# Kernel tuning notes

Measured on AMD Instinct MI355X. Metric: run time of the kernel, lower is better.

## Reference

```python
import jax, jax.numpy as jnp
import numpy as np

N_NODES = 20000
N_EDGES = 320000
N_ADJ = 4
D = 256
CSTR = [0, 1]          # constrained adjacency subset for the last step
RATIO = 1.0
LN_EPS = 1e-5


def setup_inputs() -> dict:
    key = jax.random.key(0)
    ks = jax.random.split(key, 10)
    x = jax.random.normal(ks[0], (N_NODES, D), dtype=jnp.float32)
    rows = jax.random.randint(ks[1], (N_ADJ, N_EDGES), 0, N_NODES)
    cols = jax.random.randint(ks[2], (N_ADJ, N_EDGES), 0, N_NODES)
    vals = jax.random.uniform(ks[3], (N_ADJ, N_EDGES), dtype=jnp.float32)
    W = jax.random.normal(ks[4], (D, D), dtype=jnp.float32) * (1.0 / np.sqrt(D))
    b = jax.random.normal(ks[5], (D,), dtype=jnp.float32) * 0.02
    ws_seq_0 = jax.random.uniform(ks[6], (2, N_ADJ - 1), dtype=jnp.float32)
    ws_seq_1 = jax.random.uniform(ks[7], (len(CSTR),), dtype=jnp.float32)
    ws_res_0 = jax.random.uniform(ks[8], (1, N_ADJ), dtype=jnp.float32)
    ws_res_1 = jax.random.uniform(ks[9], (2, len(CSTR) + 1), dtype=jnp.float32)
    return {"x": x, "rows": rows, "cols": cols, "vals": vals, "W": W, "b": b,
            "ws_seq_0": ws_seq_0, "ws_seq_1": ws_seq_1,
            "ws_res_0": ws_res_0, "ws_res_1": ws_res_1}


def reference(x, rows, cols, vals, W, b, ws_seq_0, ws_seq_1, ws_res_0, ws_res_1):
    n_nodes = x.shape[0]

    def spmm(a, h):
        # sparse [n,n] @ h : gather source features, scale, scatter-add by row
        return jax.ops.segment_sum(vals[a][:, None] * h[cols[a]], rows[a],
                                   num_segments=n_nodes)

    def op(h, adj_ids, w):
        # Op with k=1: random.sample selects ALL operators -> weighted mean
        acc = w[0] * spmm(adj_ids[0], h)
        for j, a in enumerate(adj_ids[1:], start=1):
            acc = acc + w[j] * spmm(a, h)
        return acc / len(adj_ids)

    h = x @ W + b                      # affine: [n_nodes, D]
    states = [h]
    # step i=0: seq only (res sum over states[:0] is empty -> 0), edge == 1
    s1 = op(states[0], [0, 1, 2], ws_seq_0[0])          # adjs[:-1]
    states.append(s1)
    # step i=1: seq on states[1] over adjs[:-1], res on states[0] over all adjs
    s2 = op(states[1], [0, 1, 2], ws_seq_0[1]) + RATIO * op(states[0], [0, 1, 2, 3], ws_res_0[0])
    states.append(s2)
    # last step: cstr adjacencies for seq; cstr + last adj for residuals
    out_seq = op(states[2], CSTR, ws_seq_1)
    res_ids = CSTR + [N_ADJ - 1]
    out_res = op(states[0], res_ids, ws_res_1[0]) + op(states[1], res_ids, ws_res_1[1])
    out = out_seq + RATIO * out_res
    # LayerNorm without affine params
    mu = jnp.mean(out, axis=-1, keepdims=True)
    var = jnp.var(out, axis=-1, keepdims=True)
    out = (out - mu) * jax.lax.rsqrt(var + LN_EPS)
    return jax.nn.gelu(out, approximate=False)
```

## Files before the change

kernel.cpp:

```cpp
#include <hip/hip_runtime.h>
#include <hip/hip_bf16.h>

#define N_NODES 20000
#define N_EDGES 320000
#define N_ADJ   4
#define D       256
#define DH      128
#define RPA     20004

#define NBUCK   79
#define NGRP    40
#define EPB     8000
#define GCAP    192
#define BMAX    4736
#define MMBLK   1250

typedef __attribute__((ext_vector_type(8))) short bf8;
typedef __attribute__((ext_vector_type(4))) float f4;


__device__ __forceinline__ unsigned f2bf_bits(float x) {
    unsigned u = __float_as_uint(x);
    return (u + 0x7FFFu + ((u >> 16) & 1u)) >> 16;
}
__device__ __forceinline__ unsigned pack_bf2(float lo, float hi) {
    return f2bf_bits(lo) | (f2bf_bits(hi) << 16);
}
__device__ __forceinline__ float bf_lo(unsigned p) { return __uint_as_float(p << 16); }
__device__ __forceinline__ float bf_hi(unsigned p) { return __uint_as_float(p & 0xFFFF0000u); }


__global__ __launch_bounds__(1024) void prep_kernel(const int* __restrict__ rows,
                                                    const int* __restrict__ cols,
                                                    const float* __restrict__ vals,
                                                    int* __restrict__ cnt,
                                                    uint2* __restrict__ stage,
                                                    const float* __restrict__ W,
                                                    uint4* __restrict__ wh,
                                                    uint4* __restrict__ wl) {
    __shared__ int lcnt[NBUCK];
    int g = blockIdx.x, a = blockIdx.y, t = threadIdx.x;

    if (g >= NGRP) {
        if (a != 0) return;
        for (int i = (g - NGRP) * 1024 + t; i < 8192; i += 2048) {
            int lane = i & 63;
            int tile = i >> 6;
            int ks = tile >> 4, n = tile & 15;
            int m = lane & 15, quad = lane >> 4;
            int col = n * 16 + m;
            int k0  = ks * 32 + quad * 8;
            unsigned hbits[8], lbits[8];
            #pragma unroll
            for (int j = 0; j < 8; ++j) {
                float v = W[(k0 + j) * D + col];
                unsigned hb = f2bf_bits(v);
                float lo = v - __uint_as_float(hb << 16);
                hbits[j] = hb;
                lbits[j] = f2bf_bits(lo);
            }
            uint4 hh, ll;
            hh.x = hbits[0] | (hbits[1] << 16); hh.y = hbits[2] | (hbits[3] << 16);
            hh.z = hbits[4] | (hbits[5] << 16); hh.w = hbits[6] | (hbits[7] << 16);
            ll.x = lbits[0] | (lbits[1] << 16); ll.y = lbits[2] | (lbits[3] << 16);
            ll.z = lbits[4] | (lbits[5] << 16); ll.w = lbits[6] | (lbits[7] << 16);
            wh[i] = hh;
            wl[i] = ll;
        }
        return;
    }

    if (t < NBUCK) lcnt[t] = 0;
    __syncthreads();
    int e0 = g * EPB;
    #pragma unroll 1
    for (int i = 0; i < EPB; i += 1024) {
        int e = e0 + i + t;
        if (i + t < EPB) {
            int r   = rows[a * N_EDGES + e];
            int c   = cols[a * N_EDGES + e];
            float v = vals[a * N_EDGES + e];
            int b   = r >> 8;
            int idx = atomicAdd(&lcnt[b], 1);
            if (idx < GCAP) {
                stage[(size_t)((a * NBUCK + b) * NGRP + g) * GCAP + idx] =
                    make_uint2((f2bf_bits(v) << 16) | (unsigned)c, (unsigned)(r & 255));
            }
        }
    }
    __syncthreads();
    if (t < NBUCK) cnt[(a * NBUCK + t) * NGRP + g] = min(lcnt[t], GCAP);
}


__global__ __launch_bounds__(256) void buildmm_kernel(const float* __restrict__ x,
                                                      const uint4* __restrict__ wh,
                                                      const uint4* __restrict__ wl,
                                                      const float* __restrict__ bvec,
                                                      unsigned* __restrict__ hp,
                                                      const int* __restrict__ cnt,
                                                      const uint2* __restrict__ stage,
                                                      unsigned* __restrict__ csr,
                                                      int* __restrict__ row_ptr) {
    __shared__ uint2 recs[BMAX];
    __shared__ int scn[256];
    __shared__ int offs[256];
    __shared__ int gbase_s;
    int t = threadIdx.x;

    if (blockIdx.x < MMBLK) {
        int wid = t >> 6, lane = t & 63;
        int r0 = blockIdx.x * 16;
        int m = lane & 15, quad = lane >> 4;

        const float* xr = x + (size_t)(r0 + m) * D + quad * 8;
        bf8 ah[8], al[8];
        #pragma unroll
        for (int ks = 0; ks < 8; ++ks) {
            float4 v0 = *(const float4*)(xr + ks * 32);
            float4 v1 = *(const float4*)(xr + ks * 32 + 4);
            float xs[8] = {v0.x, v0.y, v0.z, v0.w, v1.x, v1.y, v1.z, v1.w};
            #pragma unroll
            for (int j = 0; j < 8; ++j) {
                unsigned hb = f2bf_bits(xs[j]);
                float lo = xs[j] - __uint_as_float(hb << 16);
                ah[ks][j] = (short)hb;
                al[ks][j] = (short)f2bf_bits(lo);
            }
        }

        #pragma unroll
        for (int i = 0; i < 4; ++i) {
            int n = wid * 4 + i;
            f4 c = {0.f, 0.f, 0.f, 0.f};
            #pragma unroll
            for (int ks = 0; ks < 8; ++ks) {
                uint4 bh4 = wh[(ks * 16 + n) * 64 + lane];
                uint4 bl4 = wl[(ks * 16 + n) * 64 + lane];
                bf8 bh = *(bf8*)&bh4;
                bf8 bl = *(bf8*)&bl4;
                c = __builtin_amdgcn_mfma_f32_16x16x32_bf16(ah[ks], bh, c, 0, 0, 0);
                c = __builtin_amdgcn_mfma_f32_16x16x32_bf16(al[ks], bh, c, 0, 0, 0);
                c = __builtin_amdgcn_mfma_f32_16x16x32_bf16(ah[ks], bl, c, 0, 0, 0);
            }
            int col = n * 16 + m;
            float bb = bvec[col];
            #pragma unroll
            for (int reg = 0; reg < 4; ++reg) {
                float v = c[reg] + bb;
                float o = __shfl_xor(v, 1, 64);
                if ((m & 1) == 0) {
                    hp[(r0 + quad * 4 + reg) * DH + (col >> 1)] = pack_bf2(v, o);
                }
            }
        }
        return;
    }

    int linear = blockIdx.x - MMBLK;
    int a = linear / NBUCK, b = linear % NBUCK;

    if (t == 0) gbase_s = 0;
    __syncthreads();
    int part = 0;
    for (int i = t; i < b * NGRP; i += 256) part += cnt[a * (NBUCK * NGRP) + i];
    #pragma unroll
    for (int off = 32; off > 0; off >>= 1) part += __shfl_xor(part, off, 64);
    if ((t & 63) == 0) atomicAdd(&gbase_s, part);

    int goff = 0;
    #pragma unroll 1
    for (int g = 0; g < NGRP; ++g) {
        int c = cnt[(a * NBUCK + b) * NGRP + g];
        const uint2* src = stage + (size_t)((a * NBUCK + b) * NGRP + g) * GCAP;
        for (int i = t; i < c; i += 256) {
            int d = goff + i;
            if (d < BMAX) recs[d] = src[i];
        }
        goff += c;
    }
    int total = min(goff, BMAX);

    scn[t] = 0;
    offs[t] = 0;
    __syncthreads();
    for (int i = t; i < total; i += 256) atomicAdd(&scn[recs[i].y], 1);
    __syncthreads();
    int mycnt = scn[t];
    for (int off = 1; off < 256; off <<= 1) {
        int add = (t >= off) ? scn[t - off] : 0;
        __syncthreads();
        scn[t] += add;
        __syncthreads();
    }
    int excl = scn[t] - mycnt;
    __syncthreads();
    scn[t] = excl;
    __syncthreads();

    int gbase = gbase_s;
    for (int i = t; i < total; i += 256) {
        int lr  = recs[i].y;
        int pos = scn[lr] + atomicAdd(&offs[lr], 1);
        csr[(size_t)a * N_EDGES + gbase + pos] = recs[i].x;
    }
    int r = b * 256 + t;
    if (r <= N_NODES) row_ptr[(size_t)a * RPA + r] = gbase + excl;
}


__device__ __forceinline__ void gather_seg(const unsigned* __restrict__ E, int beg, int end,
                                           const uint2* __restrict__ feat2, int lane,
                                           float* __restrict__ s ) {
    int n = end - beg;
    const unsigned* e = E + beg;
    int m8 = n & ~7;
    if (m8) {
        unsigned rec[8];
        #pragma unroll
        for (int j = 0; j < 8; ++j) rec[j] = e[j];
        for (int i = 8; ; i += 8) {
            uint2 p[8];
            #pragma unroll
            for (int j = 0; j < 8; ++j)
                p[j] = feat2[((rec[j] & 0xFFFFu) << 6) + lane];
            bool more = i < m8;
            unsigned nrec[8];
            if (more) {
                #pragma unroll
                for (int j = 0; j < 8; ++j) nrec[j] = e[i + j];
            }
            #pragma unroll
            for (int j = 0; j < 8; ++j) {
                float v = __uint_as_float(rec[j] & 0xFFFF0000u);
                s[0] += v * bf_lo(p[j].x);
                s[1] += v * bf_hi(p[j].x);
                s[2] += v * bf_lo(p[j].y);
                s[3] += v * bf_hi(p[j].y);
            }
            if (!more) break;
            #pragma unroll
            for (int j = 0; j < 8; ++j) rec[j] = nrec[j];
        }
    }
    for (int i = m8; i < n; ++i) {
        unsigned rr = e[i];
        uint2 pp = feat2[((rr & 0xFFFFu) << 6) + lane];
        float vv = __uint_as_float(rr & 0xFFFF0000u);
        s[0] += vv * bf_lo(pp.x);
        s[1] += vv * bf_hi(pp.x);
        s[2] += vv * bf_lo(pp.y);
        s[3] += vv * bf_hi(pp.y);
    }
}


__global__ __launch_bounds__(256) void stage1_kernel(const uint2* __restrict__ hp2,
                                                     const int* __restrict__ row_ptr,
                                                     const unsigned* __restrict__ csr,
                                                     const float* __restrict__ wseq0,
                                                     const float* __restrict__ wres0,
                                                     const float* __restrict__ wres1,
                                                     uint2* __restrict__ s1p2,
                                                     uint2* __restrict__ s2p2,
                                                     float4* __restrict__ outp4) {
    int t = threadIdx.x, wid = t >> 6, lane = t & 63;
    int r = blockIdx.x * 4 + wid;
    float acc[N_ADJ][4];
    #pragma unroll
    for (int a = 0; a < N_ADJ; ++a) {
        acc[a][0] = acc[a][1] = acc[a][2] = acc[a][3] = 0.f;
        const int* rp = row_ptr + (size_t)a * RPA;
        int beg = __builtin_amdgcn_readfirstlane(rp[r]);
        int end = __builtin_amdgcn_readfirstlane(rp[r + 1]);
        gather_seg(csr + (size_t)a * N_EDGES, beg, end, hp2, lane, acc[a]);
    }
    const float third = 1.f / 3.f;
    float w0 = wseq0[0] * third, w1 = wseq0[1] * third, w2 = wseq0[2] * third;
    float q0 = wres0[0] * 0.25f, q1 = wres0[1] * 0.25f, q2 = wres0[2] * 0.25f, q3 = wres0[3] * 0.25f;
    float u0 = wres1[0] * third, u1 = wres1[1] * third, u2 = wres1[2] * third;
    float s1v[4], s2v[4], ov[4];
    #pragma unroll
    for (int j = 0; j < 4; ++j) {
        s1v[j] = w0 * acc[0][j] + w1 * acc[1][j] + w2 * acc[2][j];
        s2v[j] = q0 * acc[0][j] + q1 * acc[1][j] + q2 * acc[2][j] + q3 * acc[3][j];
        ov[j]  = u0 * acc[0][j] + u1 * acc[1][j] + u2 * acc[3][j];
    }
    int o = r * 64 + lane;
    s1p2[o]  = make_uint2(pack_bf2(s1v[0], s1v[1]), pack_bf2(s1v[2], s1v[3]));
    s2p2[o]  = make_uint2(pack_bf2(s2v[0], s2v[1]), pack_bf2(s2v[2], s2v[3]));
    outp4[o] = make_float4(ov[0], ov[1], ov[2], ov[3]);
}


__global__ __launch_bounds__(256) void stage2_kernel(const uint2* __restrict__ s1p2,
                                                     const int* __restrict__ row_ptr,
                                                     const unsigned* __restrict__ csr,
                                                     const float* __restrict__ wseq0,
                                                     const float* __restrict__ wres1,
                                                     uint2* __restrict__ s2p2,
                                                     float4* __restrict__ outp4) {
    int t = threadIdx.x, wid = t >> 6, lane = t & 63;
    int r = blockIdx.x * 4 + wid;
    float acc[N_ADJ][4];
    #pragma unroll
    for (int a = 0; a < N_ADJ; ++a) {
        acc[a][0] = acc[a][1] = acc[a][2] = acc[a][3] = 0.f;
        const int* rp = row_ptr + (size_t)a * RPA;
        int beg = __builtin_amdgcn_readfirstlane(rp[r]);
        int end = __builtin_amdgcn_readfirstlane(rp[r + 1]);
        gather_seg(csr + (size_t)a * N_EDGES, beg, end, s1p2, lane, acc[a]);
    }
    const float third = 1.f / 3.f;
    float w3 = wseq0[3] * third, w4 = wseq0[4] * third, w5 = wseq0[5] * third;
    float u3 = wres1[3] * third, u4 = wres1[4] * third, u5 = wres1[5] * third;
    int o = r * 64 + lane;
    uint2 sp = s2p2[o];
    float c0 = bf_lo(sp.x) + w3 * acc[0][0] + w4 * acc[1][0] + w5 * acc[2][0];
    float c1 = bf_hi(sp.x) + w3 * acc[0][1] + w4 * acc[1][1] + w5 * acc[2][1];
    float c2 = bf_lo(sp.y) + w3 * acc[0][2] + w4 * acc[1][2] + w5 * acc[2][2];
    float c3 = bf_hi(sp.y) + w3 * acc[0][3] + w4 * acc[1][3] + w5 * acc[2][3];
    s2p2[o] = make_uint2(pack_bf2(c0, c1), pack_bf2(c2, c3));
    float4 op = outp4[o];
    op.x += u3 * acc[0][0] + u4 * acc[1][0] + u5 * acc[3][0];
    op.y += u3 * acc[0][1] + u4 * acc[1][1] + u5 * acc[3][1];
    op.z += u3 * acc[0][2] + u4 * acc[1][2] + u5 * acc[3][2];
    op.w += u3 * acc[0][3] + u4 * acc[1][3] + u5 * acc[3][3];
    outp4[o] = op;
}


__global__ __launch_bounds__(256) void stage3_kernel(const uint2* __restrict__ s2p2,
                                                     const int* __restrict__ row_ptr,
                                                     const unsigned* __restrict__ csr,
                                                     const float* __restrict__ wseq1,
                                                     float4* __restrict__ outp4) {
    int t = threadIdx.x, wid = t >> 6, lane = t & 63;
    int r = blockIdx.x * 4 + wid;
    float acc[2][4];
    #pragma unroll
    for (int a = 0; a < 2; ++a) {
        acc[a][0] = acc[a][1] = acc[a][2] = acc[a][3] = 0.f;
        const int* rp = row_ptr + (size_t)a * RPA;
        int beg = __builtin_amdgcn_readfirstlane(rp[r]);
        int end = __builtin_amdgcn_readfirstlane(rp[r + 1]);
        gather_seg(csr + (size_t)a * N_EDGES, beg, end, s2p2, lane, acc[a]);
    }
    float e0 = wseq1[0] * 0.5f, e1 = wseq1[1] * 0.5f;
    int o = r * 64 + lane;
    float4 op = outp4[o];
    float v0 = op.x + e0 * acc[0][0] + e1 * acc[1][0];
    float v1 = op.y + e0 * acc[0][1] + e1 * acc[1][1];
    float v2 = op.z + e0 * acc[0][2] + e1 * acc[1][2];
    float v3 = op.w + e0 * acc[0][3] + e1 * acc[1][3];

    float sv = v0 + v1 + v2 + v3;
    float sq = v0 * v0 + v1 * v1 + v2 * v2 + v3 * v3;
    #pragma unroll
    for (int off = 32; off > 0; off >>= 1) {
        sv += __shfl_xor(sv, off, 64);
        sq += __shfl_xor(sq, off, 64);
    }
    float mu   = sv * (1.f / 256.f);
    float var  = sq * (1.f / 256.f) - mu * mu;
    float rstd = rsqrtf(var + 1e-5f);
    float y0 = (v0 - mu) * rstd;
    float y1 = (v1 - mu) * rstd;
    float y2 = (v2 - mu) * rstd;
    float y3 = (v3 - mu) * rstd;
    const float is2 = 0.70710678118654752440f;
    outp4[o] = make_float4(0.5f * y0 * (1.f + erff(y0 * is2)),
                           0.5f * y1 * (1.f + erff(y1 * is2)),
                           0.5f * y2 * (1.f + erff(y2 * is2)),
                           0.5f * y3 * (1.f + erff(y3 * is2)));
}


extern "C" void kernel_launch(void* const* d_in, const int* in_sizes, int n_in,
                              void* d_out, int out_size, void* d_ws, size_t ws_size,
                              hipStream_t stream) {
    const float* x     = (const float*)d_in[0];
    const int*   rows  = (const int*)d_in[1];
    const int*   cols  = (const int*)d_in[2];
    const float* vals  = (const float*)d_in[3];
    const float* W     = (const float*)d_in[4];
    const float* b     = (const float*)d_in[5];
    const float* wseq0 = (const float*)d_in[6];
    const float* wseq1 = (const float*)d_in[7];
    const float* wres0 = (const float*)d_in[8];
    const float* wres1 = (const float*)d_in[9];
    float4* outp4 = (float4*)d_out;

    char* p = (char*)d_ws;
    unsigned* hp  = (unsigned*)p; p += (size_t)N_NODES * DH * 4;
    unsigned* s1p = (unsigned*)p; p += (size_t)N_NODES * DH * 4;
    unsigned* s2p = (unsigned*)p; p += (size_t)N_NODES * DH * 4;
    int* row_ptr  = (int*)p;      p += (size_t)N_ADJ * RPA * 4;
    int* cnt      = (int*)p;      p += (N_ADJ * NBUCK * NGRP * 4 + 127) / 128 * 128;
    uint4* wh     = (uint4*)p;    p += 8192 * 16;
    uint4* wl     = (uint4*)p;    p += 8192 * 16;
    unsigned* csr = (unsigned*)p;
    uint2* stage  = (uint2*)s1p;

    prep_kernel<<<dim3(NGRP + 2, N_ADJ), 1024, 0, stream>>>(rows, cols, vals, cnt,
                                                            stage, W, wh, wl);
    buildmm_kernel<<<MMBLK + NBUCK * N_ADJ, 256, 0, stream>>>(x, wh, wl, b, hp,
                                                              cnt, stage, csr, row_ptr);

    stage1_kernel<<<N_NODES / 4, 256, 0, stream>>>((const uint2*)hp, row_ptr, csr,
                                                   wseq0, wres0, wres1,
                                                   (uint2*)s1p, (uint2*)s2p, outp4);
    stage2_kernel<<<N_NODES / 4, 256, 0, stream>>>((const uint2*)s1p, row_ptr, csr,
                                                   wseq0, wres1, (uint2*)s2p, outp4);
    stage3_kernel<<<N_NODES / 4, 256, 0, stream>>>((const uint2*)s2p, row_ptr, csr,
                                                   wseq1, outp4);
}
```

Baseline: 329.3 us.

## Sub-sort CSR rows by source-column quarter and gather quarter-by-quarter across adjacencies

New measurement: 352.8 us. 1.07x slower.

```diff
diff --git a/kernel.cpp b/kernel.cpp
--- a/kernel.cpp
+++ b/kernel.cpp
@@ -6,7 +6,7 @@
 #define N_ADJ   4
 #define D       256
 #define DH      128
-#define RPA     20004
+#define RP4A    80016
 
 #define NBUCK   79
 #define NGRP    40
@@ -15,8 +15,11 @@
 #define BMAX    4736
 #define MMBLK   1250
 
+#define GD      4
+
 typedef __attribute__((ext_vector_type(8))) short bf8;
 typedef __attribute__((ext_vector_type(4))) float f4;
+typedef __attribute__((ext_vector_type(2))) unsigned u2v;
 
 
 __device__ __forceinline__ unsigned f2bf_bits(float x) {
@@ -83,8 +86,10 @@
             int b   = r >> 8;
             int idx = atomicAdd(&lcnt[b], 1);
             if (idx < GCAP) {
+                unsigned q = (unsigned)((c >= 5000) + (c >= 10000) + (c >= 15000));
                 stage[(size_t)((a * NBUCK + b) * NGRP + g) * GCAP + idx] =
-                    make_uint2((f2bf_bits(v) << 16) | (unsigned)c, (unsigned)(r & 255));
+                    make_uint2((f2bf_bits(v) << 16) | (unsigned)c,
+                               (unsigned)((r & 255) * 4) + q);
             }
         }
     }
@@ -101,10 +106,11 @@
                                                       const int* __restrict__ cnt,
                                                       const uint2* __restrict__ stage,
                                                       unsigned* __restrict__ csr,
-                                                      int* __restrict__ row_ptr) {
+                                                      int* __restrict__ rp4) {
     __shared__ uint2 recs[BMAX];
-    __shared__ int scn[256];
-    __shared__ int offs[256];
+    __shared__ int scn[1024];
+    __shared__ int offs[1024];
+    __shared__ int tscan[256];
     __shared__ int gbase_s;
     int t = threadIdx.x;
 
@@ -181,82 +187,91 @@
     }
     int total = min(goff, BMAX);
 
-    scn[t] = 0;
-    offs[t] = 0;
+    #pragma unroll
+    for (int k = 0; k < 4; ++k) { scn[t * 4 + k] = 0; offs[t * 4 + k] = 0; }
     __syncthreads();
     for (int i = t; i < total; i += 256) atomicAdd(&scn[recs[i].y], 1);
     __syncthreads();
-    int mycnt = scn[t];
+    int c0 = scn[t * 4], c1 = scn[t * 4 + 1], c2 = scn[t * 4 + 2], c3 = scn[t * 4 + 3];
+    int tsum = c0 + c1 + c2 + c3;
+    tscan[t] = tsum;
+    __syncthreads();
     for (int off = 1; off < 256; off <<= 1) {
-        int add = (t >= off) ? scn[t - off] : 0;
+        int add = (t >= off) ? tscan[t - off] : 0;
         __syncthreads();
-        scn[t] += add;
+        tscan[t] += add;
         __syncthreads();
     }
-    int excl = scn[t] - mycnt;
-    __syncthreads();
-    scn[t] = excl;
+    int texcl = tscan[t] - tsum;
+    int e0 = texcl, e1 = e0 + c0, e2 = e1 + c1, e3 = e2 + c2;
+    scn[t * 4] = e0; scn[t * 4 + 1] = e1; scn[t * 4 + 2] = e2; scn[t * 4 + 3] = e3;
     __syncthreads();
 
     int gbase = gbase_s;
     for (int i = t; i < total; i += 256) {
-        int lr  = recs[i].y;
-        int pos = scn[lr] + atomicAdd(&offs[lr], 1);
+        int key = recs[i].y;
+        int pos = scn[key] + atomicAdd(&offs[key], 1);
         csr[(size_t)a * N_EDGES + gbase + pos] = recs[i].x;
     }
     int r = b * 256 + t;
-    if (r <= N_NODES) row_ptr[(size_t)a * RPA + r] = gbase + excl;
+    if (r <= N_NODES) {
+        rp4[(size_t)a * RP4A + r * 4 + 0] = gbase + e0;
+        rp4[(size_t)a * RP4A + r * 4 + 1] = gbase + e1;
+        rp4[(size_t)a * RP4A + r * 4 + 2] = gbase + e2;
+        rp4[(size_t)a * RP4A + r * 4 + 3] = gbase + e3;
+    }
 }
 
 
 __device__ __forceinline__ void gather_seg(const unsigned* __restrict__ E, int beg, int end,
-                                           const uint2* __restrict__ feat2, int lane,
+                                           const uint2* __restrict__ feat2, int lo8 ,
                                            float* __restrict__ s ) {
     int n = end - beg;
+    if (n <= 0) return;
     const unsigned* e = E + beg;
-    int m8 = n & ~7;
-    if (m8) {
-        unsigned rec[8];
-        #pragma unroll
-        for (int j = 0; j < 8; ++j) rec[j] = e[j];
-        for (int i = 8; ; i += 8) {
-            uint2 p[8];
+    int lim = n - 1;
+    unsigned rec[GD];
+    #pragma unroll
+    for (int j = 0; j < GD; ++j) rec[j] = e[min(j, lim)];
+    int base = 0;
+    #pragma unroll 1
+    for (;;) {
+        u2v p[GD];
+        #pragma unroll
+        for (int j = 0; j < GD; ++j) {
+            unsigned voff = ((rec[j] & 0xFFFFu) << 9) + (unsigned)lo8;
+            asm volatile("global_load_dwordx2 %0, %1, %2"
+                         : "=v"(p[j])
+                         : "v"(voff), "s"(feat2));
+        }
+        int nbase = base + GD;
+        bool more = nbase < n;
+        unsigned nrec[GD];
+        if (more) {
             #pragma unroll
-            for (int j = 0; j < 8; ++j)
-                p[j] = feat2[((rec[j] & 0xFFFFu) << 6) + lane];
-            bool more = i < m8;
-            unsigned nrec[8];
-            if (more) {
-                #pragma unroll
-                for (int j = 0; j < 8; ++j) nrec[j] = e[i + j];
-            }
-            #pragma unroll
-            for (int j = 0; j < 8; ++j) {
-                float v = __uint_as_float(rec[j] & 0xFFFF0000u);
-                s[0] += v * bf_lo(p[j].x);
-                s[1] += v * bf_hi(p[j].x);
-                s[2] += v * bf_lo(p[j].y);
-                s[3] += v * bf_hi(p[j].y);
-            }
-            if (!more) break;
-            #pragma unroll
-            for (int j = 0; j < 8; ++j) rec[j] = nrec[j];
-        }
-    }
-    for (int i = m8; i < n; ++i) {
-        unsigned rr = e[i];
-        uint2 pp = feat2[((rr & 0xFFFFu) << 6) + lane];
-        float vv = __uint_as_float(rr & 0xFFFF0000u);
-        s[0] += vv * bf_lo(pp.x);
-        s[1] += vv * bf_hi(pp.x);
-        s[2] += vv * bf_lo(pp.y);
-        s[3] += vv * bf_hi(pp.y);
+            for (int j = 0; j < GD; ++j) nrec[j] = e[min(nbase + j, lim)];
+        }
+        asm volatile("s_waitcnt vmcnt(0)"
+                     : "+v"(p[0]), "+v"(p[1]), "+v"(p[2]), "+v"(p[3]));
+        #pragma unroll
+        for (int j = 0; j < GD; ++j) {
+            unsigned vb = (base + j <= lim) ? (rec[j] & 0xFFFF0000u) : 0u;
+            float v = __uint_as_float(vb);
+            s[0] += v * bf_lo(p[j][0]);
+            s[1] += v * bf_hi(p[j][0]);
+            s[2] += v * bf_lo(p[j][1]);
+            s[3] += v * bf_hi(p[j][1]);
+        }
+        if (!more) break;
+        #pragma unroll
+        for (int j = 0; j < GD; ++j) rec[j] = nrec[j];
+        base = nbase;
     }
 }
 
 
 __global__ __launch_bounds__(256) void stage1_kernel(const uint2* __restrict__ hp2,
-                                                     const int* __restrict__ row_ptr,
+                                                     const int* __restrict__ rp4,
                                                      const unsigned* __restrict__ csr,
                                                      const float* __restrict__ wseq0,
                                                      const float* __restrict__ wres0,
@@ -266,15 +281,25 @@
                                                      float4* __restrict__ outp4) {
     int t = threadIdx.x, wid = t >> 6, lane = t & 63;
     int r = blockIdx.x * 4 + wid;
+    int lo8 = lane * 8;
+    int rps[N_ADJ][5];
+    #pragma unroll
+    for (int a = 0; a < N_ADJ; ++a)
+        #pragma unroll
+        for (int k = 0; k < 5; ++k)
+            rps[a][k] = __builtin_amdgcn_readfirstlane(rp4[(size_t)a * RP4A + r * 4 + k]);
+
     float acc[N_ADJ][4];
     #pragma unroll
-    for (int a = 0; a < N_ADJ; ++a) {
+    for (int a = 0; a < N_ADJ; ++a)
         acc[a][0] = acc[a][1] = acc[a][2] = acc[a][3] = 0.f;
-        const int* rp = row_ptr + (size_t)a * RPA;
-        int beg = __builtin_amdgcn_readfirstlane(rp[r]);
-        int end = __builtin_amdgcn_readfirstlane(rp[r + 1]);
-        gather_seg(csr + (size_t)a * N_EDGES, beg, end, hp2, lane, acc[a]);
-    }
+
+    #pragma unroll
+    for (int q = 0; q < 4; ++q)
+        #pragma unroll
+        for (int a = 0; a < N_ADJ; ++a)
+            gather_seg(csr + (size_t)a * N_EDGES, rps[a][q], rps[a][q + 1], hp2, lo8, acc[a]);
+
     const float third = 1.f / 3.f;
     float w0 = wseq0[0] * third, w1 = wseq0[1] * third, w2 = wseq0[2] * third;
     float q0 = wres0[0] * 0.25f, q1 = wres0[1] * 0.25f, q2 = wres0[2] * 0.25f, q3 = wres0[3] * 0.25f;
@@ -294,7 +319,7 @@
 
 
 __global__ __launch_bounds__(256) void stage2_kernel(const uint2* __restrict__ s1p2,
-                                                     const int* __restrict__ row_ptr,
+                                                     const int* __restrict__ rp4,
                                                      const unsigned* __restrict__ csr,
                                                      const float* __restrict__ wseq0,
                                                      const float* __restrict__ wres1,
@@ -302,15 +327,25 @@
                                                      float4* __restrict__ outp4) {
     int t = threadIdx.x, wid = t >> 6, lane = t & 63;
     int r = blockIdx.x * 4 + wid;
+    int lo8 = lane * 8;
+    int rps[N_ADJ][5];
+    #pragma unroll
+    for (int a = 0; a < N_ADJ; ++a)
+        #pragma unroll
+        for (int k = 0; k < 5; ++k)
+            rps[a][k] = __builtin_amdgcn_readfirstlane(rp4[(size_t)a * RP4A + r * 4 + k]);
+
     float acc[N_ADJ][4];
     #pragma unroll
-    for (int a = 0; a < N_ADJ; ++a) {
+    for (int a = 0; a < N_ADJ; ++a)
         acc[a][0] = acc[a][1] = acc[a][2] = acc[a][3] = 0.f;
-        const int* rp = row_ptr + (size_t)a * RPA;
-        int beg = __builtin_amdgcn_readfirstlane(rp[r]);
-        int end = __builtin_amdgcn_readfirstlane(rp[r + 1]);
-        gather_seg(csr + (size_t)a * N_EDGES, beg, end, s1p2, lane, acc[a]);
-    }
+
+    #pragma unroll
+    for (int q = 0; q < 4; ++q)
+        #pragma unroll
+        for (int a = 0; a < N_ADJ; ++a)
+            gather_seg(csr + (size_t)a * N_EDGES, rps[a][q], rps[a][q + 1], s1p2, lo8, acc[a]);
+
     const float third = 1.f / 3.f;
     float w3 = wseq0[3] * third, w4 = wseq0[4] * third, w5 = wseq0[5] * third;
     float u3 = wres1[3] * third, u4 = wres1[4] * third, u5 = wres1[5] * third;
@@ -331,21 +366,31 @@
 
 
 __global__ __launch_bounds__(256) void stage3_kernel(const uint2* __restrict__ s2p2,
-                                                     const int* __restrict__ row_ptr,
+                                                     const int* __restrict__ rp4,
                                                      const unsigned* __restrict__ csr,
                                                      const float* __restrict__ wseq1,
                                                      float4* __restrict__ outp4) {
     int t = threadIdx.x, wid = t >> 6, lane = t & 63;
     int r = blockIdx.x * 4 + wid;
+    int lo8 = lane * 8;
+    int rps[2][5];
+    #pragma unroll
+    for (int a = 0; a < 2; ++a)
+        #pragma unroll
+        for (int k = 0; k < 5; ++k)
+            rps[a][k] = __builtin_amdgcn_readfirstlane(rp4[(size_t)a * RP4A + r * 4 + k]);
+
     float acc[2][4];
     #pragma unroll
-    for (int a = 0; a < 2; ++a) {
+    for (int a = 0; a < 2; ++a)
         acc[a][0] = acc[a][1] = acc[a][2] = acc[a][3] = 0.f;
-        const int* rp = row_ptr + (size_t)a * RPA;
-        int beg = __builtin_amdgcn_readfirstlane(rp[r]);
-        int end = __builtin_amdgcn_readfirstlane(rp[r + 1]);
-        gather_seg(csr + (size_t)a * N_EDGES, beg, end, s2p2, lane, acc[a]);
-    }
+
+    #pragma unroll
+    for (int q = 0; q < 4; ++q)
+        #pragma unroll
+        for (int a = 0; a < 2; ++a)
+            gather_seg(csr + (size_t)a * N_EDGES, rps[a][q], rps[a][q + 1], s2p2, lo8, acc[a]);
+
     float e0 = wseq1[0] * 0.5f, e1 = wseq1[1] * 0.5f;
     int o = r * 64 + lane;
     float4 op = outp4[o];
@@ -395,7 +440,7 @@
     unsigned* hp  = (unsigned*)p; p += (size_t)N_NODES * DH * 4;
     unsigned* s1p = (unsigned*)p; p += (size_t)N_NODES * DH * 4;
     unsigned* s2p = (unsigned*)p; p += (size_t)N_NODES * DH * 4;
-    int* row_ptr  = (int*)p;      p += (size_t)N_ADJ * RPA * 4;
+    int* rp4      = (int*)p;      p += (size_t)N_ADJ * RP4A * 4;
     int* cnt      = (int*)p;      p += (N_ADJ * NBUCK * NGRP * 4 + 127) / 128 * 128;
     uint4* wh     = (uint4*)p;    p += 8192 * 16;
     uint4* wl     = (uint4*)p;    p += 8192 * 16;
@@ -405,13 +450,13 @@
     prep_kernel<<<dim3(NGRP + 2, N_ADJ), 1024, 0, stream>>>(rows, cols, vals, cnt,
                                                             stage, W, wh, wl);
     buildmm_kernel<<<MMBLK + NBUCK * N_ADJ, 256, 0, stream>>>(x, wh, wl, b, hp,
-                                                              cnt, stage, csr, row_ptr);
-
-    stage1_kernel<<<N_NODES / 4, 256, 0, stream>>>((const uint2*)hp, row_ptr, csr,
+                                                              cnt, stage, csr, rp4);
+
+    stage1_kernel<<<N_NODES / 4, 256, 0, stream>>>((const uint2*)hp, rp4, csr,
                                                    wseq0, wres0, wres1,
                                                    (uint2*)s1p, (uint2*)s2p, outp4);
-    stage2_kernel<<<N_NODES / 4, 256, 0, stream>>>((const uint2*)s1p, row_ptr, csr,
+    stage2_kernel<<<N_NODES / 4, 256, 0, stream>>>((const uint2*)s1p, rp4, csr,
                                                    wseq0, wres1, (uint2*)s2p, outp4);
-    stage3_kernel<<<N_NODES / 4, 256, 0, stream>>>((const uint2*)s2p, row_ptr, csr,
+    stage3_kernel<<<N_NODES / 4, 256, 0, stream>>>((const uint2*)s2p, rp4, csr,
                                                    wseq1, outp4);
 }
```

## Split feature tables into column planes and gather per plane with quarter-wave edges

Applied to the files above, without the earlier changes.

Measured after the change: 454.7 us. 38.1% more time.

```diff
diff --git a/kernel.cpp b/kernel.cpp
--- a/kernel.cpp
+++ b/kernel.cpp
@@ -7,6 +7,8 @@
 #define D       256
 #define DH      128
 #define RPA     20004
+#define PLANE_DW 640000
+#define PLANE_U2 320000
 
 #define NBUCK   79
 #define NGRP    40
@@ -150,7 +152,10 @@
                 float v = c[reg] + bb;
                 float o = __shfl_xor(v, 1, 64);
                 if ((m & 1) == 0) {
-                    hp[(r0 + quad * 4 + reg) * DH + (col >> 1)] = pack_bf2(v, o);
+                    int pl = col >> 6;
+                    int dw = (col >> 1) & 31;
+                    hp[(size_t)pl * PLANE_DW + (r0 + quad * 4 + reg) * 32 + dw] =
+                        pack_bf2(v, o);
                 }
             }
         }
@@ -209,63 +214,48 @@
 }
 
 
-__device__ __forceinline__ void gather_seg(const unsigned* __restrict__ E, int beg, int end,
-                                           const uint2* __restrict__ feat2, int lane,
-                                           float* __restrict__ s ) {
+__device__ __forceinline__ void gather_q(const unsigned* __restrict__ e, int beg, int end,
+                                         const unsigned* __restrict__ plane,
+                                         int sub, int fl, float* __restrict__ s) {
     int n = end - beg;
-    const unsigned* e = E + beg;
-    int m8 = n & ~7;
-    if (m8) {
-        unsigned rec[8];
-        #pragma unroll
-        for (int j = 0; j < 8; ++j) rec[j] = e[j];
-        for (int i = 8; ; i += 8) {
-            uint2 p[8];
-            #pragma unroll
-            for (int j = 0; j < 8; ++j)
-                p[j] = feat2[((rec[j] & 0xFFFFu) << 6) + lane];
-            bool more = i < m8;
-            unsigned nrec[8];
-            if (more) {
-                #pragma unroll
-                for (int j = 0; j < 8; ++j) nrec[j] = e[i + j];
-            }
-            #pragma unroll
-            for (int j = 0; j < 8; ++j) {
-                float v = __uint_as_float(rec[j] & 0xFFFF0000u);
-                s[0] += v * bf_lo(p[j].x);
-                s[1] += v * bf_hi(p[j].x);
-                s[2] += v * bf_lo(p[j].y);
-                s[3] += v * bf_hi(p[j].y);
-            }
-            if (!more) break;
-            #pragma unroll
-            for (int j = 0; j < 8; ++j) rec[j] = nrec[j];
-        }
-    }
-    for (int i = m8; i < n; ++i) {
-        unsigned rr = e[i];
-        uint2 pp = feat2[((rr & 0xFFFFu) << 6) + lane];
-        float vv = __uint_as_float(rr & 0xFFFF0000u);
-        s[0] += vv * bf_lo(pp.x);
-        s[1] += vv * bf_hi(pp.x);
-        s[2] += vv * bf_lo(pp.y);
-        s[3] += vv * bf_hi(pp.y);
-    }
-}
-
-
-__global__ __launch_bounds__(256) void stage1_kernel(const uint2* __restrict__ hp2,
+    const unsigned* ee = e + beg;
+    int lim = n - 1;
+    #pragma unroll 2
+    for (int base = 0; base < n; base += 4) {
+        int idx = base + sub;
+        unsigned rec = ee[min(idx, lim)];
+        unsigned vb = (idx <= lim) ? (rec & 0xFFFF0000u) : 0u;
+        float v = __uint_as_float(vb);
+        uint2 p = *((const uint2*)(plane + (size_t)(rec & 0xFFFFu) * 32) + fl);
+        s[0] += v * bf_lo(p.x);
+        s[1] += v * bf_hi(p.x);
+        s[2] += v * bf_lo(p.y);
+        s[3] += v * bf_hi(p.y);
+    }
+}
+
+__device__ __forceinline__ float red4(float v) {
+    v += __shfl_xor(v, 16, 64);
+    v += __shfl_xor(v, 32, 64);
+    return v;
+}
+
+
+__global__ __launch_bounds__(256) void stage1_kernel(const unsigned* __restrict__ hp,
                                                      const int* __restrict__ row_ptr,
                                                      const unsigned* __restrict__ csr,
                                                      const float* __restrict__ wseq0,
                                                      const float* __restrict__ wres0,
                                                      const float* __restrict__ wres1,
-                                                     uint2* __restrict__ s1p2,
-                                                     uint2* __restrict__ s2p2,
-                                                     float4* __restrict__ outp4) {
+                                                     unsigned* __restrict__ s1p,
+                                                     unsigned* __restrict__ s2p,
+                                                     float4* __restrict__ outp4,
+                                                     int q) {
     int t = threadIdx.x, wid = t >> 6, lane = t & 63;
+    int sub = lane >> 4, fl = lane & 15;
     int r = blockIdx.x * 4 + wid;
+    const unsigned* plane = hp + (size_t)q * PLANE_DW;
+
     float acc[N_ADJ][4];
     #pragma unroll
     for (int a = 0; a < N_ADJ; ++a) {
@@ -273,7 +263,7 @@
         const int* rp = row_ptr + (size_t)a * RPA;
         int beg = __builtin_amdgcn_readfirstlane(rp[r]);
         int end = __builtin_amdgcn_readfirstlane(rp[r + 1]);
-        gather_seg(csr + (size_t)a * N_EDGES, beg, end, hp2, lane, acc[a]);
+        gather_q(csr + (size_t)a * N_EDGES, beg, end, plane, sub, fl, acc[a]);
     }
     const float third = 1.f / 3.f;
     float w0 = wseq0[0] * third, w1 = wseq0[1] * third, w2 = wseq0[2] * third;
@@ -282,26 +272,32 @@
     float s1v[4], s2v[4], ov[4];
     #pragma unroll
     for (int j = 0; j < 4; ++j) {
-        s1v[j] = w0 * acc[0][j] + w1 * acc[1][j] + w2 * acc[2][j];
-        s2v[j] = q0 * acc[0][j] + q1 * acc[1][j] + q2 * acc[2][j] + q3 * acc[3][j];
-        ov[j]  = u0 * acc[0][j] + u1 * acc[1][j] + u2 * acc[3][j];
-    }
-    int o = r * 64 + lane;
-    s1p2[o]  = make_uint2(pack_bf2(s1v[0], s1v[1]), pack_bf2(s1v[2], s1v[3]));
-    s2p2[o]  = make_uint2(pack_bf2(s2v[0], s2v[1]), pack_bf2(s2v[2], s2v[3]));
-    outp4[o] = make_float4(ov[0], ov[1], ov[2], ov[3]);
-}
-
-
-__global__ __launch_bounds__(256) void stage2_kernel(const uint2* __restrict__ s1p2,
+        s1v[j] = red4(w0 * acc[0][j] + w1 * acc[1][j] + w2 * acc[2][j]);
+        s2v[j] = red4(q0 * acc[0][j] + q1 * acc[1][j] + q2 * acc[2][j] + q3 * acc[3][j]);
+        ov[j]  = red4(u0 * acc[0][j] + u1 * acc[1][j] + u2 * acc[3][j]);
+    }
+    if (sub == 0) {
+        int o2 = q * PLANE_U2 + r * 16 + fl;
+        ((uint2*)s1p)[o2] = make_uint2(pack_bf2(s1v[0], s1v[1]), pack_bf2(s1v[2], s1v[3]));
+        ((uint2*)s2p)[o2] = make_uint2(pack_bf2(s2v[0], s2v[1]), pack_bf2(s2v[2], s2v[3]));
+        outp4[r * 64 + q * 16 + fl] = make_float4(ov[0], ov[1], ov[2], ov[3]);
+    }
+}
+
+
+__global__ __launch_bounds__(256) void stage2_kernel(const unsigned* __restrict__ s1p,
                                                      const int* __restrict__ row_ptr,
                                                      const unsigned* __restrict__ csr,
                                                      const float* __restrict__ wseq0,
                                                      const float* __restrict__ wres1,
-                                                     uint2* __restrict__ s2p2,
-                                                     float4* __restrict__ outp4) {
+                                                     unsigned* __restrict__ s2p,
+                                                     float4* __restrict__ outp4,
+                                                     int q) {
     int t = threadIdx.x, wid = t >> 6, lane = t & 63;
+    int sub = lane >> 4, fl = lane & 15;
     int r = blockIdx.x * 4 + wid;
+    const unsigned* plane = s1p + (size_t)q * PLANE_DW;
+
     float acc[N_ADJ][4];
     #pragma unroll
     for (int a = 0; a < N_ADJ; ++a) {
@@ -309,34 +305,43 @@
         const int* rp = row_ptr + (size_t)a * RPA;
         int beg = __builtin_amdgcn_readfirstlane(rp[r]);
         int end = __builtin_amdgcn_readfirstlane(rp[r + 1]);
-        gather_seg(csr + (size_t)a * N_EDGES, beg, end, s1p2, lane, acc[a]);
+        gather_q(csr + (size_t)a * N_EDGES, beg, end, plane, sub, fl, acc[a]);
     }
     const float third = 1.f / 3.f;
     float w3 = wseq0[3] * third, w4 = wseq0[4] * third, w5 = wseq0[5] * third;
     float u3 = wres1[3] * third, u4 = wres1[4] * third, u5 = wres1[5] * third;
-    int o = r * 64 + lane;
-    uint2 sp = s2p2[o];
-    float c0 = bf_lo(sp.x) + w3 * acc[0][0] + w4 * acc[1][0] + w5 * acc[2][0];
-    float c1 = bf_hi(sp.x) + w3 * acc[0][1] + w4 * acc[1][1] + w5 * acc[2][1];
-    float c2 = bf_lo(sp.y) + w3 * acc[0][2] + w4 * acc[1][2] + w5 * acc[2][2];
-    float c3 = bf_hi(sp.y) + w3 * acc[0][3] + w4 * acc[1][3] + w5 * acc[2][3];
-    s2p2[o] = make_uint2(pack_bf2(c0, c1), pack_bf2(c2, c3));
-    float4 op = outp4[o];
-    op.x += u3 * acc[0][0] + u4 * acc[1][0] + u5 * acc[3][0];
-    op.y += u3 * acc[0][1] + u4 * acc[1][1] + u5 * acc[3][1];
-    op.z += u3 * acc[0][2] + u4 * acc[1][2] + u5 * acc[3][2];
-    op.w += u3 * acc[0][3] + u4 * acc[1][3] + u5 * acc[3][3];
-    outp4[o] = op;
-}
-
-
-__global__ __launch_bounds__(256) void stage3_kernel(const uint2* __restrict__ s2p2,
+    float cs[4], os[4];
+    #pragma unroll
+    for (int j = 0; j < 4; ++j) {
+        cs[j] = red4(w3 * acc[0][j] + w4 * acc[1][j] + w5 * acc[2][j]);
+        os[j] = red4(u3 * acc[0][j] + u4 * acc[1][j] + u5 * acc[3][j]);
+    }
+    if (sub == 0) {
+        int o2 = q * PLANE_U2 + r * 16 + fl;
+        uint2 sp = ((uint2*)s2p)[o2];
+        float c0 = bf_lo(sp.x) + cs[0];
+        float c1 = bf_hi(sp.x) + cs[1];
+        float c2 = bf_lo(sp.y) + cs[2];
+        float c3 = bf_hi(sp.y) + cs[3];
+        ((uint2*)s2p)[o2] = make_uint2(pack_bf2(c0, c1), pack_bf2(c2, c3));
+        float4 op = outp4[r * 64 + q * 16 + fl];
+        op.x += os[0]; op.y += os[1]; op.z += os[2]; op.w += os[3];
+        outp4[r * 64 + q * 16 + fl] = op;
+    }
+}
+
+
+__global__ __launch_bounds__(256) void stage3_kernel(const unsigned* __restrict__ s2p,
                                                      const int* __restrict__ row_ptr,
                                                      const unsigned* __restrict__ csr,
                                                      const float* __restrict__ wseq1,
-                                                     float4* __restrict__ outp4) {
+                                                     float4* __restrict__ outp4,
+                                                     int q) {
     int t = threadIdx.x, wid = t >> 6, lane = t & 63;
+    int sub = lane >> 4, fl = lane & 15;
     int r = blockIdx.x * 4 + wid;
+    const unsigned* plane = s2p + (size_t)q * PLANE_DW;
+
     float acc[2][4];
     #pragma unroll
     for (int a = 0; a < 2; ++a) {
@@ -344,15 +349,26 @@
         const int* rp = row_ptr + (size_t)a * RPA;
         int beg = __builtin_amdgcn_readfirstlane(rp[r]);
         int end = __builtin_amdgcn_readfirstlane(rp[r + 1]);
-        gather_seg(csr + (size_t)a * N_EDGES, beg, end, s2p2, lane, acc[a]);
+        gather_q(csr + (size_t)a * N_EDGES, beg, end, plane, sub, fl, acc[a]);
     }
     float e0 = wseq1[0] * 0.5f, e1 = wseq1[1] * 0.5f;
-    int o = r * 64 + lane;
-    float4 op = outp4[o];
-    float v0 = op.x + e0 * acc[0][0] + e1 * acc[1][0];
-    float v1 = op.y + e0 * acc[0][1] + e1 * acc[1][1];
-    float v2 = op.z + e0 * acc[0][2] + e1 * acc[1][2];
-    float v3 = op.w + e0 * acc[0][3] + e1 * acc[1][3];
+    float vs[4];
+    #pragma unroll
+    for (int j = 0; j < 4; ++j)
+        vs[j] = red4(e0 * acc[0][j] + e1 * acc[1][j]);
+    if (sub == 0) {
+        float4 op = outp4[r * 64 + q * 16 + fl];
+        op.x += vs[0]; op.y += vs[1]; op.z += vs[2]; op.w += vs[3];
+        outp4[r * 64 + q * 16 + fl] = op;
+    }
+}
+
+
+__global__ __launch_bounds__(256) void ln_kernel(float4* __restrict__ outp4) {
+    int t = threadIdx.x, wid = t >> 6, lane = t & 63;
+    int r = blockIdx.x * 4 + wid;
+    float4 op = outp4[r * 64 + lane];
+    float v0 = op.x, v1 = op.y, v2 = op.z, v3 = op.w;
 
     float sv = v0 + v1 + v2 + v3;
     float sq = v0 * v0 + v1 * v1 + v2 * v2 + v3 * v3;
@@ -369,10 +385,10 @@
     float y2 = (v2 - mu) * rstd;
     float y3 = (v3 - mu) * rstd;
     const float is2 = 0.70710678118654752440f;
-    outp4[o] = make_float4(0.5f * y0 * (1.f + erff(y0 * is2)),
-                           0.5f * y1 * (1.f + erff(y1 * is2)),
-                           0.5f * y2 * (1.f + erff(y2 * is2)),
-                           0.5f * y3 * (1.f + erff(y3 * is2)));
+    outp4[r * 64 + lane] = make_float4(0.5f * y0 * (1.f + erff(y0 * is2)),
+                                       0.5f * y1 * (1.f + erff(y1 * is2)),
+                                       0.5f * y2 * (1.f + erff(y2 * is2)),
+                                       0.5f * y3 * (1.f + erff(y3 * is2)));
 }
 
 
@@ -407,11 +423,15 @@
     buildmm_kernel<<<MMBLK + NBUCK * N_ADJ, 256, 0, stream>>>(x, wh, wl, b, hp,
                                                               cnt, stage, csr, row_ptr);
 
-    stage1_kernel<<<N_NODES / 4, 256, 0, stream>>>((const uint2*)hp, row_ptr, csr,
-                                                   wseq0, wres0, wres1,
-                                                   (uint2*)s1p, (uint2*)s2p, outp4);
-    stage2_kernel<<<N_NODES / 4, 256, 0, stream>>>((const uint2*)s1p, row_ptr, csr,
-                                                   wseq0, wres1, (uint2*)s2p, outp4);
-    stage3_kernel<<<N_NODES / 4, 256, 0, stream>>>((const uint2*)s2p, row_ptr, csr,
-                                                   wseq1, outp4);
-}
+    for (int q = 0; q < 4; ++q)
+        stage1_kernel<<<N_NODES / 4, 256, 0, stream>>>(hp, row_ptr, csr,
+                                                       wseq0, wres0, wres1,
+                                                       s1p, s2p, outp4, q);
+    for (int q = 0; q < 4; ++q)
+        stage2_kernel<<<N_NODES / 4, 256, 0, stream>>>(s1p, row_ptr, csr,
+                                                       wseq0, wres1, s2p, outp4, q);
+    for (int q = 0; q < 4; ++q)
+        stage3_kernel<<<N_NODES / 4, 256, 0, stream>>>(s2p, row_ptr, csr,
+                                                       wseq1, outp4, q);
+    ln_kernel<<<N_NODES / 4, 256, 0, stream>>>(outp4);
+}
```

## Drop LDS record staging in bucket sort and schedule sort blocks first

Applied to the files above, without the earlier changes.

Result: faster. 310.8 us (-5.6%).

```diff
diff --git a/kernel.cpp b/kernel.cpp
--- a/kernel.cpp
+++ b/kernel.cpp
@@ -12,7 +12,7 @@
 #define NGRP    40
 #define EPB     8000
 #define GCAP    192
-#define BMAX    4736
+#define NBSORT  (NBUCK * N_ADJ)
 #define MMBLK   1250
 
 typedef __attribute__((ext_vector_type(8))) short bf8;
@@ -73,7 +73,6 @@
     if (t < NBUCK) lcnt[t] = 0;
     __syncthreads();
     int e0 = g * EPB;
-    #pragma unroll 1
     for (int i = 0; i < EPB; i += 1024) {
         int e = e0 + i + t;
         if (i + t < EPB) {
@@ -93,24 +92,24 @@
 }
 
 
-__global__ __launch_bounds__(256) void buildmm_kernel(const float* __restrict__ x,
-                                                      const uint4* __restrict__ wh,
-                                                      const uint4* __restrict__ wl,
-                                                      const float* __restrict__ bvec,
-                                                      unsigned* __restrict__ hp,
-                                                      const int* __restrict__ cnt,
-                                                      const uint2* __restrict__ stage,
-                                                      unsigned* __restrict__ csr,
-                                                      int* __restrict__ row_ptr) {
-    __shared__ uint2 recs[BMAX];
+__global__ __launch_bounds__(256) void bsmm_kernel(const float* __restrict__ x,
+                                                   const uint4* __restrict__ wh,
+                                                   const uint4* __restrict__ wl,
+                                                   const float* __restrict__ bvec,
+                                                   unsigned* __restrict__ hp,
+                                                   const int* __restrict__ cnt,
+                                                   const uint2* __restrict__ stage,
+                                                   unsigned* __restrict__ csr,
+                                                   int* __restrict__ row_ptr) {
+    __shared__ int cbs[NGRP];
     __shared__ int scn[256];
     __shared__ int offs[256];
     __shared__ int gbase_s;
     int t = threadIdx.x;
 
-    if (blockIdx.x < MMBLK) {
+    if (blockIdx.x >= NBSORT) {
         int wid = t >> 6, lane = t & 63;
-        int r0 = blockIdx.x * 16;
+        int r0 = (blockIdx.x - NBSORT) * 16;
         int m = lane & 15, quad = lane >> 4;
 
         const float* xr = x + (size_t)(r0 + m) * D + quad * 8;
@@ -157,35 +156,29 @@
         return;
     }
 
-    int linear = blockIdx.x - MMBLK;
+    int linear = blockIdx.x;
     int a = linear / NBUCK, b = linear % NBUCK;
 
     if (t == 0) gbase_s = 0;
-    __syncthreads();
+    scn[t] = 0;
+    offs[t] = 0;
+    if (t < NGRP) cbs[t] = cnt[(a * NBUCK + b) * NGRP + t];
+    __syncthreads();
+
     int part = 0;
     for (int i = t; i < b * NGRP; i += 256) part += cnt[a * (NBUCK * NGRP) + i];
     #pragma unroll
     for (int off = 32; off > 0; off >>= 1) part += __shfl_xor(part, off, 64);
     if ((t & 63) == 0) atomicAdd(&gbase_s, part);
 
-    int goff = 0;
-    #pragma unroll 1
-    for (int g = 0; g < NGRP; ++g) {
-        int c = cnt[(a * NBUCK + b) * NGRP + g];
-        const uint2* src = stage + (size_t)((a * NBUCK + b) * NGRP + g) * GCAP;
-        for (int i = t; i < c; i += 256) {
-            int d = goff + i;
-            if (d < BMAX) recs[d] = src[i];
-        }
-        goff += c;
-    }
-    int total = min(goff, BMAX);
-
-    scn[t] = 0;
-    offs[t] = 0;
-    __syncthreads();
-    for (int i = t; i < total; i += 256) atomicAdd(&scn[recs[i].y], 1);
-    __syncthreads();
+    const uint2* sb = stage + (size_t)(a * NBUCK + b) * NGRP * GCAP;
+
+    for (int i = t; i < NGRP * GCAP; i += 256) {
+        int g = i / GCAP, idx = i - g * GCAP;
+        if (idx < cbs[g]) atomicAdd(&scn[sb[i].y], 1);
+    }
+    __syncthreads();
+
     int mycnt = scn[t];
     for (int off = 1; off < 256; off <<= 1) {
         int add = (t >= off) ? scn[t - off] : 0;
@@ -199,10 +192,13 @@
     __syncthreads();
 
     int gbase = gbase_s;
-    for (int i = t; i < total; i += 256) {
-        int lr  = recs[i].y;
-        int pos = scn[lr] + atomicAdd(&offs[lr], 1);
-        csr[(size_t)a * N_EDGES + gbase + pos] = recs[i].x;
+    for (int i = t; i < NGRP * GCAP; i += 256) {
+        int g = i / GCAP, idx = i - g * GCAP;
+        if (idx < cbs[g]) {
+            uint2 rec = sb[i];
+            int pos = scn[rec.y] + atomicAdd(&offs[rec.y], 1);
+            csr[(size_t)a * N_EDGES + gbase + pos] = rec.x;
+        }
     }
     int r = b * 256 + t;
     if (r <= N_NODES) row_ptr[(size_t)a * RPA + r] = gbase + excl;
@@ -404,8 +400,8 @@
 
     prep_kernel<<<dim3(NGRP + 2, N_ADJ), 1024, 0, stream>>>(rows, cols, vals, cnt,
                                                             stage, W, wh, wl);
-    buildmm_kernel<<<MMBLK + NBUCK * N_ADJ, 256, 0, stream>>>(x, wh, wl, b, hp,
-                                                              cnt, stage, csr, row_ptr);
+    bsmm_kernel<<<NBSORT + MMBLK, 256, 0, stream>>>(x, wh, wl, b, hp,
+                                                    cnt, stage, csr, row_ptr);
 
     stage1_kernel<<<N_NODES / 4, 256, 0, stream>>>((const uint2*)hp, row_ptr, csr,
                                                    wseq0, wres0, wres1,
```
